# Kernel tuning notes

Measured on AMD Instinct MI355X. Metric: run time of the kernel, lower is better.

Reference implementation:

```python
import jax, jax.numpy as jnp
import numpy as np

B, P, T = 32, 196, 64
E = H = A = 512
V = 32000
L = 2  # num_layers


def _p(key, shape, scale=0.05):
    return jax.random.normal(key, shape, dtype=jnp.float32) * scale


def setup_inputs() -> dict:
    key = jax.random.key(0)
    ks = jax.random.split(key, 24)
    inp = {
        "encoder_out": jax.random.normal(ks[0], (B, P, E), dtype=jnp.float32),
        "captions": jax.random.randint(ks[1], (B, T), 0, V, dtype=jnp.int32),
        # embedding table (also tied fc weight)
        "emb_W": _p(ks[2], (V, E)),
        "fc_b": jnp.zeros((V,), jnp.float32),
        # attention
        "W_enc": _p(ks[3], (E, A)), "b_enc": jnp.zeros((A,), jnp.float32),
        "W_dec": _p(ks[4], (H, A)), "b_dec": jnp.zeros((A,), jnp.float32),
        "W_full": _p(ks[5], (A, 1)), "b_full": jnp.zeros((1,), jnp.float32),
        # LSTM layer 0 (input = 2E), layer 1 (input = H); PyTorch gate order i,f,g,o
        "Wih0": _p(ks[6], (4 * H, 2 * E)), "Whh0": _p(ks[7], (4 * H, H)),
        "bih0": jnp.zeros((4 * H,), jnp.float32), "bhh0": jnp.zeros((4 * H,), jnp.float32),
        "Wih1": _p(ks[8], (4 * H, H)), "Whh1": _p(ks[9], (4 * H, H)),
        "bih1": jnp.zeros((4 * H,), jnp.float32), "bhh1": jnp.zeros((4 * H,), jnp.float32),
        # init hidden/cell projections
        "W_init_h": _p(ks[10], (E, H * L)), "b_init_h": jnp.zeros((H * L,), jnp.float32),
        "W_init_c": _p(ks[11], (E, H * L)), "b_init_c": jnp.zeros((H * L,), jnp.float32),
    }
    return inp


def _lstm_cell(x, h, c, Wih, Whh, b):
    gates = x @ Wih.T + h @ Whh.T + b  # [B, 4H]
    i, f, g, o = jnp.split(gates, 4, axis=-1)
    c_new = jax.nn.sigmoid(f) * c + jax.nn.sigmoid(i) * jnp.tanh(g)
    h_new = jax.nn.sigmoid(o) * jnp.tanh(c_new)
    return h_new, c_new


def _forward(encoder_out, captions, emb_W, fc_b, W_enc, b_enc, W_dec, b_dec,
             W_full, b_full, Wih0, Whh0, bih0, bhh0, Wih1, Whh1, bih1, bhh1,
             W_init_h, b_init_h, W_init_c, b_init_c):
    # dropout is identity (eval mode)
    Bsz = encoder_out.shape[0]
    mean_enc = encoder_out.mean(axis=1)  # [B, E]
    # PyTorch: .view(num_layers, B, -1) on a [B, H*L] tensor -> flat reshape
    h = (mean_enc @ W_init_h + b_init_h).reshape(L, Bsz, H)
    c = (mean_enc @ W_init_c + b_init_c).reshape(L, Bsz, H)

    enc_att = encoder_out @ W_enc + b_enc  # [B, P, A] (timestep-invariant, hoisted)
    embs = emb_W[captions]  # [B, T, E]
    b0 = bih0 + bhh0
    b1 = bih1 + bhh1

    def step(carry, emb_t):
        h, c = carry  # each [L, B, H]
        att2 = h[-1] @ W_dec + b_dec  # [B, A]
        e = (jax.nn.relu(enc_att + att2[:, None, :]) @ W_full)[..., 0] + b_full[0]  # [B, P]
        alpha = jax.nn.softmax(e, axis=1)
        context = jnp.einsum('bp,bpe->be', alpha, encoder_out)  # [B, E]
        x = jnp.concatenate([emb_t, context], axis=-1)  # [B, 2E]
        h0, c0 = _lstm_cell(x, h[0], c[0], Wih0, Whh0, b0)
        h1, c1 = _lstm_cell(h0, h[1], c[1], Wih1, Whh1, b1)
        out = h1 @ emb_W.T + fc_b  # tied-weight projection [B, V]
        return (jnp.stack([h0, h1]), jnp.stack([c0, c1])), out

    (_, _), outs = jax.lax.scan(step, (h, c), jnp.swapaxes(embs, 0, 1))
    return jnp.swapaxes(outs, 0, 1)  # [B, T, V]


def reference(encoder_out, captions, emb_W, fc_b, W_enc, b_enc, W_dec, b_dec,
              W_full, b_full, Wih0, Whh0, bih0, bhh0, Wih1, Whh1, bih1, bhh1,
              W_init_h, b_init_h, W_init_c, b_init_c):
    return _forward(encoder_out, captions, emb_W, fc_b, W_enc, b_enc, W_dec, b_dec,
                    W_full, b_full, Wih0, Whh0, bih0, bhh0, Wih1, Whh1, bih1, bhh1,
                    W_init_h, b_init_h, W_init_c, b_init_c)
```

## Files before the change

### kernel.cpp

```cpp
#include <hip/hip_runtime.h>

typedef unsigned short u16;
typedef __attribute__((ext_vector_type(4))) float f32x4;
typedef __attribute__((ext_vector_type(2))) float f32x2;
typedef __attribute__((ext_vector_type(8))) short short8;

#define B_ 32
#define P_ 196
#define T_ 64
#define V_ 32000
#define SLABF 17408

#define AT_LOAD(p)     __hip_atomic_load((p), __ATOMIC_RELAXED, __HIP_MEMORY_SCOPE_AGENT)
#define AT_STORE(p,v)  __hip_atomic_store((p), (v), __ATOMIC_RELAXED, __HIP_MEMORY_SCOPE_AGENT)

__device__ __forceinline__ u16 f2bf(float x){
  unsigned int u = __float_as_uint(x);
  u += 0x7FFFu + ((u >> 16) & 1u);
  return (u16)(u >> 16);
}
__device__ __forceinline__ float bf2f(u16 x){
  return __uint_as_float(((unsigned int)x) << 16);
}
__device__ __forceinline__ float sigf(float x){ return 1.0f/(1.0f + __expf(-x)); }
__device__ __forceinline__ float tanhfast(float x){
  float e = __expf(-2.0f*fabsf(x));
  float t = (1.0f - e)/(1.0f + e);
  return x >= 0.0f ? t : -t;
}


__global__ __launch_bounds__(256) void k_cvt_bf16(const float* __restrict__ s,
                                                  u16* __restrict__ d, int n8){
  int i = blockIdx.x*256 + threadIdx.x;
  if (i >= n8) return;
  const f32x4* sp = (const f32x4*)(s + (size_t)i*8);
  f32x4 a = sp[0], b = sp[1];
  short8 v;
#pragma unroll
  for (int j=0;j<4;++j){ v[j] = (short)f2bf(a[j]); v[4+j] = (short)f2bf(b[j]); }
  *(short8*)(d + (size_t)i*8) = v;
}

__global__ __launch_bounds__(256) void k_wencT(const float* __restrict__ W, u16* __restrict__ WT){
  int tid = threadIdx.x;
  int kc = tid & 63, a = blockIdx.x*4 + (tid >> 6);
  short8 v;
#pragma unroll
  for (int j=0;j<8;++j) v[j] = (short)f2bf(W[(kc*8+j)*512 + a]);
  *(short8*)(WT + a*512 + kc*8) = v;
}

__global__ __launch_bounds__(256) void k_mean(const float* __restrict__ enc, float* __restrict__ mean){
  int b = blockIdx.x, tid = threadIdx.x;
  f32x2 acc; acc.x = 0.f; acc.y = 0.f;
  for (int p=0;p<P_;++p){
    f32x2 v = *(const f32x2*)(enc + ((size_t)(b*P_+p))*512 + tid*2);
    acc.x += v.x; acc.y += v.y;
  }
  acc.x *= (1.0f/196.0f); acc.y *= (1.0f/196.0f);
  *(f32x2*)(mean + b*512 + tid*2) = acc;
}

__global__ __launch_bounds__(256) void k_init_state(const float* __restrict__ mean,
    const float* __restrict__ Wh, const float* __restrict__ bh,
    const float* __restrict__ Wc, const float* __restrict__ bc,
    float* __restrict__ h0, float* __restrict__ h1,
    float* __restrict__ c0, float* __restrict__ c1){
  int bid = blockIdx.x;
  int which = bid >> 7, r = (bid >> 2) & 31, jg = bid & 3;
  const float* W = which ? Wc : Wh;
  const float* bb = which ? bc : bh;
  __shared__ float m[512];
  for (int i=threadIdx.x; i<512; i+=256) m[i] = mean[r*512 + i];
  __syncthreads();
  int j = jg*256 + threadIdx.x;
  float acc = bb[j];
  for (int e=0;e<512;++e) acc += m[e]*W[e*1024 + j];
  int l = r >> 4;
  int bb2 = ((r & 15) << 1) | (j >> 9);
  int hh = j & 511;
  float* dst = which ? (l ? c1 : c0) : (l ? h1 : h0);
  dst[bb2*512 + hh] = acc;
}

__global__ __launch_bounds__(256) void k_fuse_w(const float* __restrict__ Wih0,
    const float* __restrict__ Whh0, const float* __restrict__ Wih1,
    const float* __restrict__ Whh1, float* __restrict__ W0f, float* __restrict__ W1f){
  int r = blockIdx.x, tid = threadIdx.x;
  if (r < 2048){
    for (int k=tid; k<1536; k+=256)
      W0f[(size_t)r*1536+k] = (k<1024) ? Wih0[(size_t)r*1024+k] : Whh0[(size_t)r*512 + (k-1024)];
  } else {
    int r1 = r - 2048;
    for (int k=tid; k<1024; k+=256)
      W1f[(size_t)r1*1024+k] = (k<512) ? Wih1[(size_t)r1*512+k] : Whh1[(size_t)r1*512 + (k-512)];
  }
}

#define LDAP 40
__global__ __launch_bounds__(256) void k_gemm_bf16(
    const u16* __restrict__ A, const u16* __restrict__ Bm,
    const float* __restrict__ bias, float* __restrict__ C, int N){
  __shared__ __align__(16) u16 As[128*LDAP];
  __shared__ __align__(16) u16 Bs[128*LDAP];
  int tid = threadIdx.x, l = tid & 63, w = tid >> 6;
  int m0 = blockIdx.x * 128, n0 = blockIdx.y * 128;
  int wm = w >> 1, wn = w & 1;
  f32x4 acc[4][4];
#pragma unroll
  for (int a=0;a<4;++a)
#pragma unroll
    for (int b=0;b<4;++b) acc[a][b] = (f32x4)0.0f;
  int srow = tid >> 2, schunk = tid & 3;
  const u16* gA = A + (size_t)(m0 + srow)*512 + schunk*8;
  const u16* gB = Bm + (size_t)(n0 + srow)*512 + schunk*8;
  int lr = l & 15, lk = (l >> 4) * 8;
  for (int k0 = 0; k0 < 512; k0 += 32){
    short8 va0 = *(const short8*)(gA + k0);
    short8 va1 = *(const short8*)(gA + (size_t)64*512 + k0);
    short8 vb0 = *(const short8*)(gB + k0);
    short8 vb1 = *(const short8*)(gB + (size_t)64*512 + k0);
    __syncthreads();
    *(short8*)(As + srow*LDAP + schunk*8) = va0;
    *(short8*)(As + (64+srow)*LDAP + schunk*8) = va1;
    *(short8*)(Bs + srow*LDAP + schunk*8) = vb0;
    *(short8*)(Bs + (64+srow)*LDAP + schunk*8) = vb1;
    __syncthreads();
    short8 af[4], bfv[4];
#pragma unroll
    for (int mt=0; mt<4; ++mt) af[mt]  = *(const short8*)(As + (wm*64 + mt*16 + lr)*LDAP + lk);
#pragma unroll
    for (int nt=0; nt<4; ++nt) bfv[nt] = *(const short8*)(Bs + (wn*64 + nt*16 + lr)*LDAP + lk);
#pragma unroll
    for (int mt=0; mt<4; ++mt)
#pragma unroll
      for (int nt=0; nt<4; ++nt)
        acc[mt][nt] = __builtin_amdgcn_mfma_f32_16x16x32_bf16(af[mt], bfv[nt], acc[mt][nt], 0, 0, 0);
  }
#pragma unroll
  for (int mt=0; mt<4; ++mt){
    int row = m0 + wm*64 + mt*16 + ((l >> 4) << 2);
#pragma unroll
    for (int nt=0; nt<4; ++nt){
      int col = n0 + wn*64 + nt*16 + (l & 15);
      float bv = bias[col];
#pragma unroll
      for (int j=0;j<4;++j)
        C[(size_t)(row + j)*N + col] = acc[mt][nt][j] + bv;
    }
  }
}


struct RA {
  const float* enc; const int* caps; const float* embW;
  const u16* WdecBF; const float* bdec; const float* Wfull; const float* bfull;
  const u16* encattBF; const float* W0f; const float* W1f;
  const float* bih0; const float* bhh0; const float* bih1; const float* bhh1;
  float* h0g; float* h1g; float* att2g; float* ctxg;
  const float* c0init; const float* c1init;
  u16* h1_all; int* sync;
};

__device__ __forceinline__ void gbar(int* sync, int gen){
  __syncthreads();
  int tid = threadIdx.x;
  if (tid == 0) AT_STORE(&sync[blockIdx.x*32], gen);
  if (tid < 256 && tid != blockIdx.x){
    while (AT_LOAD(&sync[tid*32]) < gen) __builtin_amdgcn_s_sleep(4);
  }
  __syncthreads();
  asm volatile("" ::: "memory");
}

__global__ __launch_bounds__(512) void k_recur(RA a){
  int bid = blockIdx.x, tid = threadIdx.x;
  int lane = tid & 63, wv = tid >> 6;
  __shared__ __align__(16) float w0s[12288];
  __shared__ __align__(16) float w1s[8192];
  __shared__ float red[2048];
  __shared__ float c0s[64], c1s[64];
  __shared__ float SinvS;
  __shared__ int capl[32];

  int xcd = bid & 7;
  int ab = xcd*4 + ((bid >> 3) & 3);
  int as = bid >> 5, c0col = as*64;
  int bb = tid >> 4, ksg = tid & 15;

  for (int idx = tid; idx < 12288; idx += 512){
    int r = idx / 1536, rem = idx - r*1536;
    int ch = rem >> 9, rem2 = rem & 511;
    int q = rem2 >> 6, rem3 = rem2 & 63;
    int ks = rem3 >> 2, e = rem3 & 3;
    int grow = (r >> 1)*512 + bid*2 + (r & 1);
    w0s[idx] = a.W0f[(size_t)grow*1536 + ch*512 + ks*32 + q*4 + e];
  }
  for (int idx = tid; idx < 8192; idx += 512){
    int r = idx >> 10, rem = idx & 1023;
    int ch = rem >> 9, rem2 = rem & 511;
    int q = rem2 >> 6, rem3 = rem2 & 63;
    int ks = rem3 >> 2, e = rem3 & 3;
    int grow = (r >> 1)*512 + bid*2 + (r & 1);
    w1s[idx] = a.W1f[(size_t)grow*1024 + ch*512 + ks*32 + q*4 + e];
  }
  if (tid < 64){
    int ci = tid >> 5, b = tid & 31, cell = bid*2 + ci;
    c0s[ci*32+b] = a.c0init[b*512 + cell];
    c1s[ci*32+b] = a.c1init[b*512 + cell];
  }
  __syncthreads();

  for (int t = 0; t < T_; ++t){
    const float* h1_rd = a.h1g + (size_t)t*SLABF;
    const float* h0_rd = a.h0g + (size_t)t*SLABF;
    float*       h0_wr = a.h0g + (size_t)(t+1)*SLABF;
    float*       h1_wr = a.h1g + (size_t)(t+1)*SLABF;
    float*       at_wr = a.att2g + (size_t)t*SLABF;
    const float* at_rd = at_wr;
    float*       cx_wr = a.ctxg + (size_t)t*SLABF;
    const float* cx_rd = cx_wr;
    int genb = t*4;

    {
      float* h1s = red; float* gp = red + 512;
      h1s[tid] = h1_rd[ab*512 + tid];
      __syncthreads();
      int c = lane, ksx = wv;
      float accp = 0.f;
      const u16* wpd = a.WdecBF + (size_t)(ksx*64)*512 + c0col + c;
#pragma unroll 8
      for (int i=0;i<64;++i) accp = fmaf(h1s[ksx*64+i], bf2f(wpd[(size_t)i*512]), accp);
      gp[ksx*64+c] = accp;
      __syncthreads();
      if (tid < 64){
        float s = a.bdec[c0col+tid];
#pragma unroll
        for (int k=0;k<8;++k) s += gp[k*64+tid];
        AT_STORE(&at_wr[ab*512 + c0col + tid], s);
      }
    }
    gbar(a.sync, genb+1);

    {
      float* att2s = red; float* gp3 = red + 512; float* alph = red + 1024;
      att2s[tid] = at_rd[ab*512 + tid];
      __syncthreads();
      float a2[8], wf[8];
#pragma unroll
      for (int j=0;j<8;++j){ a2[j] = att2s[lane*8+j]; wf[j] = a.Wfull[lane*8+j]; }
      float bf0 = a.bfull[0];
      int np = (wv < 4) ? 25 : 24;
      for (int i=0;i<np;++i){
        int p = wv + i*8;
        const u16* ep = a.encattBF + ((size_t)(ab*P_ + p))*512 + lane*8;
        short8 ev = *(const short8*)ep;
        float s = 0.f;
#pragma unroll
        for (int j=0;j<8;++j)
          s += fmaxf(bf2f((u16)ev[j]) + a2[j], 0.f) * wf[j];
#pragma unroll
        for (int o=32;o>=1;o>>=1) s += __shfl_xor(s, o);
        if (lane == 0) alph[p] = __expf(s + bf0);
      }
      __syncthreads();
      if (wv == 0){
        float v = 0.f;
#pragma unroll
        for (int i=0;i<4;++i){ int p = lane + 64*i; if (p < P_) v += alph[p]; }
#pragma unroll
        for (int o=32;o>=1;o>>=1) v += __shfl_xor(v, o);
        if (lane == 0) SinvS = 1.0f / v;
      }
      int c = lane, pk = wv;
      float accp = 0.f;
      for (int i=0;i<25;++i){
        int p = pk + 8*i;
        if (p < P_) accp = fmaf(alph[p], a.enc[((size_t)(ab*P_ + p))*512 + c0col + c], accp);
      }
      gp3[pk*64+c] = accp;
      __syncthreads();
      if (tid < 64){
        float s = 0.f;
#pragma unroll
        for (int k=0;k<8;++k) s += gp3[k*64+tid];
        AT_STORE(&cx_wr[ab*512 + c0col + tid], s * SinvS);
      }
    }
    gbar(a.sync, genb+2);

    {
      if (tid < 32) capl[tid] = a.caps[tid*T_ + t];
      __syncthreads();
      float acc[8];
#pragma unroll
      for (int r=0;r<8;++r) acc[r] = 0.f;
#pragma unroll
      for (int ch=0; ch<3; ++ch){
        const float* src;
        if (ch == 0)      src = a.embW + (size_t)capl[bb]*512 + ksg*32;
        else if (ch == 1) src = cx_rd + bb*512 + ksg*32;
        else              src = h0_rd + bb*512 + ksg*32;
        f32x4 x[8];
#pragma unroll
        for (int q=0;q<8;++q) x[q] = *(const f32x4*)(src + q*4);
        const float* wb = w0s + ch*512 + ksg*4;
#pragma unroll
        for (int q=0;q<8;++q){
          f32x4 xq = x[q];
#pragma unroll
          for (int r=0;r<8;++r){
            f32x4 w4 = *(const f32x4*)(wb + r*1536 + q*64);
            acc[r] = fmaf(xq.x,w4.x, fmaf(xq.y,w4.y, fmaf(xq.z,w4.z, fmaf(xq.w,w4.w, acc[r]))));
          }
        }
      }
#pragma unroll
      for (int r=0;r<8;++r){
        float v = acc[r];
        v += __shfl_xor(v,1); v += __shfl_xor(v,2); v += __shfl_xor(v,4); v += __shfl_xor(v,8);
        acc[r] = v;
      }
      if (ksg == 0){
#pragma unroll
        for (int ci=0;ci<2;++ci){
          int cell = bid*2 + ci;
          float gi = acc[0+ci] + a.bih0[cell]        + a.bhh0[cell];
          float gf = acc[2+ci] + a.bih0[512+cell]    + a.bhh0[512+cell];
          float gg = acc[4+ci] + a.bih0[1024+cell]   + a.bhh0[1024+cell];
          float go = acc[6+ci] + a.bih0[1536+cell]   + a.bhh0[1536+cell];
          float cp = c0s[ci*32+bb];
          float cn = sigf(gf)*cp + sigf(gi)*tanhfast(gg);
          float hn = sigf(go)*tanhfast(cn);
          c0s[ci*32+bb] = cn;
          AT_STORE(&h0_wr[bb*512 + cell], hn);
        }
      }
    }
    gbar(a.sync, genb+3);

    {
      float acc[8];
#pragma unroll
      for (int r=0;r<8;++r) acc[r] = 0.f;
#pragma unroll
      for (int ch=0; ch<2; ++ch){
        const float* src = (ch == 0) ? (h0_wr + bb*512 + ksg*32)
                                     : (h1_rd + bb*512 + ksg*32);
        f32x4 x[8];
#pragma unroll
        for (int q=0;q<8;++q) x[q] = *(const f32x4*)(src + q*4);
        const float* wb = w1s + ch*512 + ksg*4;
#pragma unroll
        for (int q=0;q<8;++q){
          f32x4 xq = x[q];
#pragma unroll
          for (int r=0;r<8;++r){
            f32x4 w4 = *(const f32x4*)(wb + r*1024 + q*64);
            acc[r] = fmaf(xq.x,w4.x, fmaf(xq.y,w4.y, fmaf(xq.z,w4.z, fmaf(xq.w,w4.w, acc[r]))));
          }
        }
      }
#pragma unroll
      for (int r=0;r<8;++r){
        float v = acc[r];
        v += __shfl_xor(v,1); v += __shfl_xor(v,2); v += __shfl_xor(v,4); v += __shfl_xor(v,8);
        acc[r] = v;
      }
      if (ksg == 0){
#pragma unroll
        for (int ci=0;ci<2;++ci){
          int cell = bid*2 + ci;
          float gi = acc[0+ci] + a.bih1[cell]        + a.bhh1[cell];
          float gf = acc[2+ci] + a.bih1[512+cell]    + a.bhh1[512+cell];
          float gg = acc[4+ci] + a.bih1[1024+cell]   + a.bhh1[1024+cell];
          float go = acc[6+ci] + a.bih1[1536+cell]   + a.bhh1[1536+cell];
          float cp = c1s[ci*32+bb];
          float cn = sigf(gf)*cp + sigf(gi)*tanhfast(gg);
          float hn = sigf(go)*tanhfast(cn);
          c1s[ci*32+bb] = cn;
          AT_STORE(&h1_wr[bb*512 + cell], hn);
          a.h1_all[((size_t)(bb*T_ + t))*512 + cell] = f2bf(hn);
        }
      }
    }
    gbar(a.sync, genb+4);
  }
}


extern "C" void kernel_launch(void* const* d_in, const int* in_sizes, int n_in,
                              void* d_out, int out_size, void* d_ws, size_t ws_size,
                              hipStream_t stream){
  const float* enc   = (const float*)d_in[0];
  const int*   caps  = (const int*)d_in[1];
  const float* embW  = (const float*)d_in[2];
  const float* fc_b  = (const float*)d_in[3];
  const float* Wenc  = (const float*)d_in[4];
  const float* benc  = (const float*)d_in[5];
  const float* Wdec  = (const float*)d_in[6];
  const float* bdec  = (const float*)d_in[7];
  const float* Wfull = (const float*)d_in[8];
  const float* bfull = (const float*)d_in[9];
  const float* Wih0  = (const float*)d_in[10];
  const float* Whh0  = (const float*)d_in[11];
  const float* bih0  = (const float*)d_in[12];
  const float* bhh0  = (const float*)d_in[13];
  const float* Wih1  = (const float*)d_in[14];
  const float* Whh1  = (const float*)d_in[15];
  const float* bih1  = (const float*)d_in[16];
  const float* bhh1  = (const float*)d_in[17];
  const float* Winh  = (const float*)d_in[18];
  const float* binh  = (const float*)d_in[19];
  const float* Winc  = (const float*)d_in[20];
  const float* binc  = (const float*)d_in[21];
  float* out = (float*)d_out;

  char* wsp = (char*)d_ws;
  size_t off = 0;
  auto alloc = [&](size_t bytes)->char*{
    char* p = wsp + off;
    off += (bytes + 255) & ~(size_t)255;
    return p;
  };
  u16*   A_enc    = (u16*)  alloc((size_t)6272*512*2);
  u16*   emb_bf   = (u16*)  alloc((size_t)V_*512*2);
  u16*   WencT    = (u16*)  alloc((size_t)512*512*2);
  u16*   WdecBF   = (u16*)  alloc((size_t)512*512*2);
  float* encatt   = (float*)alloc((size_t)6272*512*4);
  u16*   encattBF = (u16*)  alloc((size_t)6272*512*2);
  float* meanb    = (float*)alloc((size_t)32*512*4);
  float* W0f      = (float*)alloc((size_t)2048*1536*4);
  float* W1f      = (float*)alloc((size_t)2048*1024*4);
  float* h0g      = (float*)alloc((size_t)65*SLABF*4);
  float* h1g      = (float*)alloc((size_t)65*SLABF*4);
  float* att2g    = (float*)alloc((size_t)65*SLABF*4);
  float* ctxg     = (float*)alloc((size_t)65*SLABF*4);
  float* c0init   = (float*)alloc(32*512*4);
  float* c1init   = (float*)alloc(32*512*4);
  u16*   h1_all   = (u16*)  alloc((size_t)2048*512*2);
  int*   syncA    = (int*)  alloc(8192*4);
  if (off > ws_size) return;

  hipMemsetAsync(syncA, 0, 8192*4, stream);
  k_cvt_bf16<<<1568, 256, 0, stream>>>(enc, A_enc, 401408);
  k_cvt_bf16<<<8000, 256, 0, stream>>>(embW, emb_bf, 2048000);
  k_cvt_bf16<<<128, 256, 0, stream>>>(Wdec, WdecBF, 32768);
  k_wencT   <<<128, 256, 0, stream>>>(Wenc, WencT);
  k_mean    <<<32, 256, 0, stream>>>(enc, meanb);
  k_init_state<<<256, 256, 0, stream>>>(meanb, Winh, binh, Winc, binc,
                                        h0g, h1g, c0init, c1init);
  k_fuse_w<<<4096, 256, 0, stream>>>(Wih0, Whh0, Wih1, Whh1, W0f, W1f);
  k_gemm_bf16<<<dim3(49, 4), 256, 0, stream>>>(A_enc, WencT, benc, encatt, 512);
  k_cvt_bf16<<<1568, 256, 0, stream>>>(encatt, encattBF, 401408);

  RA ra;
  ra.enc = enc; ra.caps = caps; ra.embW = embW;
  ra.WdecBF = WdecBF; ra.bdec = bdec; ra.Wfull = Wfull; ra.bfull = bfull;
  ra.encattBF = encattBF; ra.W0f = W0f; ra.W1f = W1f;
  ra.bih0 = bih0; ra.bhh0 = bhh0; ra.bih1 = bih1; ra.bhh1 = bhh1;
  ra.h0g = h0g; ra.h1g = h1g; ra.att2g = att2g; ra.ctxg = ctxg;
  ra.c0init = c0init; ra.c1init = c1init;
  ra.h1_all = h1_all; ra.sync = syncA;
  void* kp[] = { &ra };
  hipLaunchCooperativeKernel((const void*)k_recur, dim3(256), dim3(512), kp, 0, stream);

  k_gemm_bf16<<<dim3(16, 250), 256, 0, stream>>>(h1_all, emb_bf, fc_b, out, V_);
}
```

Measured before the change: 2.465 ms.

## Precompute off-critical-path LSTM partial gates in earlier phases, two batches per thread

The embedding part of the layer-0 gates and the h1-recurrent part of the layer-1 gates do not depend on the phase right before them. They are now computed early, in the att2 and context phases, and stored in shared memory (pa0/pa1). Only the context/h0 and h0 contributions stay on the critical path between barriers. The thread mapping also changes to 32 k-lanes by 2 batch rows per thread, so each LDS weight load is reused for two batches, and the weight smem layout is reordered to match. This shortens the serial work after gbar 2 and gbar 3 but adds work to the earlier phases and needs more registers.

```diff
diff --git a/kernel.cpp b/kernel.cpp
--- a/kernel.cpp
+++ b/kernel.cpp
@@ -180,6 +180,7 @@
   __shared__ __align__(16) float w0s[12288];
   __shared__ __align__(16) float w1s[8192];
   __shared__ float red[2048];
+  __shared__ float pa0[264], pa1[264];
   __shared__ float c0s[64], c1s[64];
   __shared__ float SinvS;
   __shared__ int capl[32];
@@ -187,23 +188,24 @@
   int xcd = bid & 7;
   int ab = xcd*4 + ((bid >> 3) & 3);
   int as = bid >> 5, c0col = as*64;
-  int bb = tid >> 4, ksg = tid & 15;
+  int bq = tid >> 5, ksg = tid & 31;
+  int b0 = bq*2, b1 = bq*2 + 1;
 
   for (int idx = tid; idx < 12288; idx += 512){
     int r = idx / 1536, rem = idx - r*1536;
     int ch = rem >> 9, rem2 = rem & 511;
-    int q = rem2 >> 6, rem3 = rem2 & 63;
+    int q = rem2 >> 7, rem3 = rem2 & 127;
     int ks = rem3 >> 2, e = rem3 & 3;
     int grow = (r >> 1)*512 + bid*2 + (r & 1);
-    w0s[idx] = a.W0f[(size_t)grow*1536 + ch*512 + ks*32 + q*4 + e];
+    w0s[idx] = a.W0f[(size_t)grow*1536 + ch*512 + ks*16 + q*4 + e];
   }
   for (int idx = tid; idx < 8192; idx += 512){
     int r = idx >> 10, rem = idx & 1023;
     int ch = rem >> 9, rem2 = rem & 511;
-    int q = rem2 >> 6, rem3 = rem2 & 63;
+    int q = rem2 >> 7, rem3 = rem2 & 127;
     int ks = rem3 >> 2, e = rem3 & 3;
     int grow = (r >> 1)*512 + bid*2 + (r & 1);
-    w1s[idx] = a.W1f[(size_t)grow*1024 + ch*512 + ks*32 + q*4 + e];
+    w1s[idx] = a.W1f[(size_t)grow*1024 + ch*512 + ks*16 + q*4 + e];
   }
   if (tid < 64){
     int ci = tid >> 5, b = tid & 31, cell = bid*2 + ci;
@@ -226,6 +228,7 @@
     {
       float* h1s = red; float* gp = red + 512;
       h1s[tid] = h1_rd[ab*512 + tid];
+      if (tid < 32) capl[tid] = a.caps[tid*T_ + t];
       __syncthreads();
       int c = lane, ksx = wv;
       float accp = 0.f;
@@ -241,6 +244,36 @@
         AT_STORE(&at_wr[ab*512 + c0col + tid], s);
       }
     }
+    {
+      float p0[8], p1[8];
+#pragma unroll
+      for (int r=0;r<8;++r){ p0[r]=0.f; p1[r]=0.f; }
+      const float* e0 = a.embW + (size_t)capl[b0]*512 + ksg*16;
+      const float* e1 = a.embW + (size_t)capl[b1]*512 + ksg*16;
+      f32x4 xa[4], xb[4];
+#pragma unroll
+      for (int q=0;q<4;++q){ xa[q] = *(const f32x4*)(e0 + q*4); xb[q] = *(const f32x4*)(e1 + q*4); }
+      const float* wb = w0s + ksg*4;
+#pragma unroll
+      for (int q=0;q<4;++q){
+        f32x4 x0 = xa[q], x1 = xb[q];
+#pragma unroll
+        for (int r=0;r<8;++r){
+          f32x4 w4 = *(const f32x4*)(wb + r*1536 + q*128);
+          p0[r] = fmaf(x0.x,w4.x, fmaf(x0.y,w4.y, fmaf(x0.z,w4.z, fmaf(x0.w,w4.w, p0[r]))));
+          p1[r] = fmaf(x1.x,w4.x, fmaf(x1.y,w4.y, fmaf(x1.z,w4.z, fmaf(x1.w,w4.w, p1[r]))));
+        }
+      }
+#pragma unroll
+      for (int r=0;r<8;++r){
+        float v0 = p0[r], v1 = p1[r];
+        v0 += __shfl_xor(v0,1); v0 += __shfl_xor(v0,2); v0 += __shfl_xor(v0,4);
+        v0 += __shfl_xor(v0,8); v0 += __shfl_xor(v0,16);
+        v1 += __shfl_xor(v1,1); v1 += __shfl_xor(v1,2); v1 += __shfl_xor(v1,4);
+        v1 += __shfl_xor(v1,8); v1 += __shfl_xor(v1,16);
+        if (ksg == 0){ pa0[r*33+b0] = v0; pa0[r*33+b1] = v1; }
+      }
+    }
     gbar(a.sync, genb+1);
 
     {
@@ -288,100 +321,161 @@
         AT_STORE(&cx_wr[ab*512 + c0col + tid], s * SinvS);
       }
     }
+    {
+      float p0[8], p1[8];
+#pragma unroll
+      for (int r=0;r<8;++r){ p0[r]=0.f; p1[r]=0.f; }
+      const float* s0 = h1_rd + b0*512 + ksg*16;
+      const float* s1 = h1_rd + b1*512 + ksg*16;
+      f32x4 xa[4], xb[4];
+#pragma unroll
+      for (int q=0;q<4;++q){ xa[q] = *(const f32x4*)(s0 + q*4); xb[q] = *(const f32x4*)(s1 + q*4); }
+      const float* wb = w1s + 512 + ksg*4;
+#pragma unroll
+      for (int q=0;q<4;++q){
+        f32x4 x0 = xa[q], x1 = xb[q];
+#pragma unroll
+        for (int r=0;r<8;++r){
+          f32x4 w4 = *(const f32x4*)(wb + r*1024 + q*128);
+          p0[r] = fmaf(x0.x,w4.x, fmaf(x0.y,w4.y, fmaf(x0.z,w4.z, fmaf(x0.w,w4.w, p0[r]))));
+          p1[r] = fmaf(x1.x,w4.x, fmaf(x1.y,w4.y, fmaf(x1.z,w4.z, fmaf(x1.w,w4.w, p1[r]))));
+        }
+      }
+#pragma unroll
+      for (int r=0;r<8;++r){
+        float v0 = p0[r], v1 = p1[r];
+        v0 += __shfl_xor(v0,1); v0 += __shfl_xor(v0,2); v0 += __shfl_xor(v0,4);
+        v0 += __shfl_xor(v0,8); v0 += __shfl_xor(v0,16);
+        v1 += __shfl_xor(v1,1); v1 += __shfl_xor(v1,2); v1 += __shfl_xor(v1,4);
+        v1 += __shfl_xor(v1,8); v1 += __shfl_xor(v1,16);
+        if (ksg == 0){ pa1[r*33+b0] = v0; pa1[r*33+b1] = v1; }
+      }
+    }
     gbar(a.sync, genb+2);
 
     {
-      if (tid < 32) capl[tid] = a.caps[tid*T_ + t];
-      __syncthreads();
-      float acc[8];
-#pragma unroll
-      for (int r=0;r<8;++r) acc[r] = 0.f;
-#pragma unroll
-      for (int ch=0; ch<3; ++ch){
-        const float* src;
-        if (ch == 0)      src = a.embW + (size_t)capl[bb]*512 + ksg*32;
-        else if (ch == 1) src = cx_rd + bb*512 + ksg*32;
-        else              src = h0_rd + bb*512 + ksg*32;
-        f32x4 x[8];
-#pragma unroll
-        for (int q=0;q<8;++q) x[q] = *(const f32x4*)(src + q*4);
-        const float* wb = w0s + ch*512 + ksg*4;
-#pragma unroll
-        for (int q=0;q<8;++q){
-          f32x4 xq = x[q];
+      float ac0[8], ac1[8];
+#pragma unroll
+      for (int r=0;r<8;++r){ ac0[r]=0.f; ac1[r]=0.f; }
+#pragma unroll
+      for (int ch=0; ch<2; ++ch){
+        const float* base = (ch == 0) ? cx_rd : h0_rd;
+        const float* s0 = base + b0*512 + ksg*16;
+        const float* s1 = base + b1*512 + ksg*16;
+        f32x4 xa[4], xb[4];
+#pragma unroll
+        for (int q=0;q<4;++q){ xa[q] = *(const f32x4*)(s0 + q*4); xb[q] = *(const f32x4*)(s1 + q*4); }
+        const float* wb = w0s + (ch+1)*512 + ksg*4;
+#pragma unroll
+        for (int q=0;q<4;++q){
+          f32x4 x0 = xa[q], x1 = xb[q];
 #pragma unroll
           for (int r=0;r<8;++r){
-            f32x4 w4 = *(const f32x4*)(wb + r*1536 + q*64);
-            acc[r] = fmaf(xq.x,w4.x, fmaf(xq.y,w4.y, fmaf(xq.z,w4.z, fmaf(xq.w,w4.w, acc[r]))));
+            f32x4 w4 = *(const f32x4*)(wb + r*1536 + q*128);
+            ac0[r] = fmaf(x0.x,w4.x, fmaf(x0.y,w4.y, fmaf(x0.z,w4.z, fmaf(x0.w,w4.w, ac0[r]))));
+            ac1[r] = fmaf(x1.x,w4.x, fmaf(x1.y,w4.y, fmaf(x1.z,w4.z, fmaf(x1.w,w4.w, ac1[r]))));
           }
         }
       }
 #pragma unroll
       for (int r=0;r<8;++r){
-        float v = acc[r];
-        v += __shfl_xor(v,1); v += __shfl_xor(v,2); v += __shfl_xor(v,4); v += __shfl_xor(v,8);
-        acc[r] = v;
+        float v0 = ac0[r], v1 = ac1[r];
+        v0 += __shfl_xor(v0,1); v0 += __shfl_xor(v0,2); v0 += __shfl_xor(v0,4);
+        v0 += __shfl_xor(v0,8); v0 += __shfl_xor(v0,16);
+        v1 += __shfl_xor(v1,1); v1 += __shfl_xor(v1,2); v1 += __shfl_xor(v1,4);
+        v1 += __shfl_xor(v1,8); v1 += __shfl_xor(v1,16);
+        ac0[r] = v0; ac1[r] = v1;
       }
       if (ksg == 0){
 #pragma unroll
         for (int ci=0;ci<2;++ci){
           int cell = bid*2 + ci;
-          float gi = acc[0+ci] + a.bih0[cell]        + a.bhh0[cell];
-          float gf = acc[2+ci] + a.bih0[512+cell]    + a.bhh0[512+cell];
-          float gg = acc[4+ci] + a.bih0[1024+cell]   + a.bhh0[1024+cell];
-          float go = acc[6+ci] + a.bih0[1536+cell]   + a.bhh0[1536+cell];
-          float cp = c0s[ci*32+bb];
-          float cn = sigf(gf)*cp + sigf(gi)*tanhfast(gg);
-          float hn = sigf(go)*tanhfast(cn);
-          c0s[ci*32+bb] = cn;
-          AT_STORE(&h0_wr[bb*512 + cell], hn);
-        }
-      }
-    }
-    gbar(a.sync, genb+3);
-
-    {
-      float acc[8];
-#pragma unroll
-      for (int r=0;r<8;++r) acc[r] = 0.f;
-#pragma unroll
-      for (int ch=0; ch<2; ++ch){
-        const float* src = (ch == 0) ? (h0_wr + bb*512 + ksg*32)
-                                     : (h1_rd + bb*512 + ksg*32);
-        f32x4 x[8];
-#pragma unroll
-        for (int q=0;q<8;++q) x[q] = *(const f32x4*)(src + q*4);
-        const float* wb = w1s + ch*512 + ksg*4;
-#pragma unroll
-        for (int q=0;q<8;++q){
-          f32x4 xq = x[q];
-#pragma unroll
-          for (int r=0;r<8;++r){
-            f32x4 w4 = *(const f32x4*)(wb + r*1024 + q*64);
-            acc[r] = fmaf(xq.x,w4.x, fmaf(xq.y,w4.y, fmaf(xq.z,w4.z, fmaf(xq.w,w4.w, acc[r]))));
+          {
+            float gi = ac0[0+ci] + pa0[(0+ci)*33+b0] + a.bih0[cell]      + a.bhh0[cell];
+            float gf = ac0[2+ci] + pa0[(2+ci)*33+b0] + a.bih0[512+cell]  + a.bhh0[512+cell];
+            float gg = ac0[4+ci] + pa0[(4+ci)*33+b0] + a.bih0[1024+cell] + a.bhh0[1024+cell];
+            float go = ac0[6+ci] + pa0[(6+ci)*33+b0] + a.bih0[1536+cell] + a.bhh0[1536+cell];
+            float cp = c0s[ci*32+b0];
+            float cn = sigf(gf)*cp + sigf(gi)*tanhfast(gg);
+            float hn = sigf(go)*tanhfast(cn);
+            c0s[ci*32+b0] = cn;
+            AT_STORE(&h0_wr[b0*512 + cell], hn);
+          }
+          {
+            float gi = ac1[0+ci] + pa0[(0+ci)*33+b1] + a.bih0[cell]      + a.bhh0[cell];
+            float gf = ac1[2+ci] + pa0[(2+ci)*33+b1] + a.bih0[512+cell]  + a.bhh0[512+cell];
+            float gg = ac1[4+ci] + pa0[(4+ci)*33+b1] + a.bih0[1024+cell] + a.bhh0[1024+cell];
+            float go = ac1[6+ci] + pa0[(6+ci)*33+b1] + a.bih0[1536+cell] + a.bhh0[1536+cell];
+            float cp = c0s[ci*32+b1];
+            float cn = sigf(gf)*cp + sigf(gi)*tanhfast(gg);
+            float hn = sigf(go)*tanhfast(cn);
+            c0s[ci*32+b1] = cn;
+            AT_STORE(&h0_wr[b1*512 + cell], hn);
           }
         }
       }
+    }
+    gbar(a.sync, genb+3);
+
+    {
+      float ac0[8], ac1[8];
+#pragma unroll
+      for (int r=0;r<8;++r){ ac0[r]=0.f; ac1[r]=0.f; }
+      {
+        const float* s0 = h0_wr + b0*512 + ksg*16;
+        const float* s1 = h0_wr + b1*512 + ksg*16;
+        f32x4 xa[4], xb[4];
+#pragma unroll
+        for (int q=0;q<4;++q){ xa[q] = *(const f32x4*)(s0 + q*4); xb[q] = *(const f32x4*)(s1 + q*4); }
+        const float* wb = w1s + ksg*4;
+#pragma unroll
+        for (int q=0;q<4;++q){
+          f32x4 x0 = xa[q], x1 = xb[q];
+#pragma unroll
+          for (int r=0;r<8;++r){
+            f32x4 w4 = *(const f32x4*)(wb + r*1024 + q*128);
+            ac0[r] = fmaf(x0.x,w4.x, fmaf(x0.y,w4.y, fmaf(x0.z,w4.z, fmaf(x0.w,w4.w, ac0[r]))));
+            ac1[r] = fmaf(x1.x,w4.x, fmaf(x1.y,w4.y, fmaf(x1.z,w4.z, fmaf(x1.w,w4.w, ac1[r]))));
+          }
+        }
+      }
 #pragma unroll
       for (int r=0;r<8;++r){
-        float v = acc[r];
-        v += __shfl_xor(v,1); v += __shfl_xor(v,2); v += __shfl_xor(v,4); v += __shfl_xor(v,8);
-        acc[r] = v;
+        float v0 = ac0[r], v1 = ac1[r];
+        v0 += __shfl_xor(v0,1); v0 += __shfl_xor(v0,2); v0 += __shfl_xor(v0,4);
+        v0 += __shfl_xor(v0,8); v0 += __shfl_xor(v0,16);
+        v1 += __shfl_xor(v1,1); v1 += __shfl_xor(v1,2); v1 += __shfl_xor(v1,4);
+        v1 += __shfl_xor(v1,8); v1 += __shfl_xor(v1,16);
+        ac0[r] = v0; ac1[r] = v1;
       }
       if (ksg == 0){
 #pragma unroll
         for (int ci=0;ci<2;++ci){
           int cell = bid*2 + ci;
-          float gi = acc[0+ci] + a.bih1[cell]        + a.bhh1[cell];
-          float gf = acc[2+ci] + a.bih1[512+cell]    + a.bhh1[512+cell];
-          float gg = acc[4+ci] + a.bih1[1024+cell]   + a.bhh1[1024+cell];
-          float go = acc[6+ci] + a.bih1[1536+cell]   + a.bhh1[1536+cell];
-          float cp = c1s[ci*32+bb];
-          float cn = sigf(gf)*cp + sigf(gi)*tanhfast(gg);
-          float hn = sigf(go)*tanhfast(cn);
-          c1s[ci*32+bb] = cn;
-          AT_STORE(&h1_wr[bb*512 + cell], hn);
-          a.h1_all[((size_t)(bb*T_ + t))*512 + cell] = f2bf(hn);
+          {
+            float gi = ac0[0+ci] + pa1[(0+ci)*33+b0] + a.bih1[cell]      + a.bhh1[cell];
+            float gf = ac0[2+ci] + pa1[(2+ci)*33+b0] + a.bih1[512+cell]  + a.bhh1[512+cell];
+            float gg = ac0[4+ci] + pa1[(4+ci)*33+b0] + a.bih1[1024+cell] + a.bhh1[1024+cell];
+            float go = ac0[6+ci] + pa1[(6+ci)*33+b0] + a.bih1[1536+cell] + a.bhh1[1536+cell];
+            float cp = c1s[ci*32+b0];
+            float cn = sigf(gf)*cp + sigf(gi)*tanhfast(gg);
+            float hn = sigf(go)*tanhfast(cn);
+            c1s[ci*32+b0] = cn;
+            AT_STORE(&h1_wr[b0*512 + cell], hn);
+            a.h1_all[((size_t)(b0*T_ + t))*512 + cell] = f2bf(hn);
+          }
+          {
+            float gi = ac1[0+ci] + pa1[(0+ci)*33+b1] + a.bih1[cell]      + a.bhh1[cell];
+            float gf = ac1[2+ci] + pa1[(2+ci)*33+b1] + a.bih1[512+cell]  + a.bhh1[512+cell];
+            float gg = ac1[4+ci] + pa1[(4+ci)*33+b1] + a.bih1[1024+cell] + a.bhh1[1024+cell];
+            float go = ac1[6+ci] + pa1[(6+ci)*33+b1] + a.bih1[1536+cell] + a.bhh1[1536+cell];
+            float cp = c1s[ci*32+b1];
+            float cn = sigf(gf)*cp + sigf(gi)*tanhfast(gg);
+            float hn = sigf(go)*tanhfast(cn);
+            c1s[ci*32+b1] = cn;
+            AT_STORE(&h1_wr[b1*512 + cell], hn);
+            a.h1_all[((size_t)(b1*T_ + t))*512 + cell] = f2bf(hn);
+          }
         }
       }
     }
```

New measurement: 2.732 ms. 10.8% more time.

## Partition recurrent kernel per batch row with 8-block group barriers and bf16 streamed weights

Applied to the files above, without the earlier changes.

The persistent recurrent kernel is restructured so each batch row is owned by a group of 8 blocks that split the hidden cells. Grid-wide 256-block barriers are replaced by 8-block group barriers. LSTM weights are packed into bf16 and streamed from global memory (L2) each step instead of being held as fp32 in LDS. The attention softmax gains a cross-block exp exchange, and context reads the bf16 encoder copy. This is meant to cut global barrier latency, but each block now rereads about 2.5 MB of weights per step and accepts extra bf16 rounding.

```diff
diff --git a/kernel.cpp b/kernel.cpp
--- a/kernel.cpp
+++ b/kernel.cpp
@@ -10,6 +10,7 @@
 #define T_ 64
 #define V_ 32000
 #define SLABF 17408
+#define EXPS  7424
 
 #define AT_LOAD(p)     __hip_atomic_load((p), __ATOMIC_RELAXED, __HIP_MEMORY_SCOPE_AGENT)
 #define AT_STORE(p,v)  __hip_atomic_store((p), (v), __ATOMIC_RELAXED, __HIP_MEMORY_SCOPE_AGENT)
@@ -84,17 +85,24 @@
   dst[bb2*512 + hh] = acc;
 }
 
-__global__ __launch_bounds__(256) void k_fuse_w(const float* __restrict__ Wih0,
+__global__ __launch_bounds__(512) void k_pack(const float* __restrict__ Wih0,
     const float* __restrict__ Whh0, const float* __restrict__ Wih1,
-    const float* __restrict__ Whh1, float* __restrict__ W0f, float* __restrict__ W1f){
-  int r = blockIdx.x, tid = threadIdx.x;
-  if (r < 2048){
-    for (int k=tid; k<1536; k+=256)
-      W0f[(size_t)r*1536+k] = (k<1024) ? Wih0[(size_t)r*1024+k] : Whh0[(size_t)r*512 + (k-1024)];
+    const float* __restrict__ Whh1, u16* __restrict__ W0bf, u16* __restrict__ W1bf){
+  int bidx = blockIdx.x, tid = threadIdx.x;
+  int ci = tid >> 3, e = tid & 7;
+  if (bidx < 6144){
+    int kc = bidx % 192, gg = bidx / 192;
+    int gate = gg & 3, g = gg >> 2;
+    int row = gate*512 + g*64 + ci, k = kc*8 + e;
+    float v = (k < 1024) ? Wih0[(size_t)row*1024 + k] : Whh0[(size_t)row*512 + (k-1024)];
+    W0bf[(size_t)bidx*512 + tid] = f2bf(v);
   } else {
-    int r1 = r - 2048;
-    for (int k=tid; k<1024; k+=256)
-      W1f[(size_t)r1*1024+k] = (k<512) ? Wih1[(size_t)r1*512+k] : Whh1[(size_t)r1*512 + (k-512)];
+    int b2 = bidx - 6144;
+    int kc = b2 % 128, gg = b2 / 128;
+    int gate = gg & 3, g = gg >> 2;
+    int row = gate*512 + g*64 + ci, k = kc*8 + e;
+    float v = (k < 512) ? Wih1[(size_t)row*512 + k] : Whh1[(size_t)row*512 + (k-512)];
+    W1bf[(size_t)b2*512 + tid] = f2bf(v);
   }
 }
 
@@ -154,63 +162,41 @@
 
 
 struct RA {
-  const float* enc; const int* caps; const float* embW;
-  const u16* WdecBF; const float* bdec; const float* Wfull; const float* bfull;
-  const u16* encattBF; const float* W0f; const float* W1f;
+  const int* caps; const float* embW; const float* Wdec; const float* bdec;
+  const float* Wfull; const float* bfull;
+  const u16* encattBF; const u16* encBF;
+  const u16* W0bf; const u16* W1bf;
   const float* bih0; const float* bhh0; const float* bih1; const float* bhh1;
-  float* h0g; float* h1g; float* att2g; float* ctxg;
+  float* h0g; float* h1g; float* att2g; float* ctxg; float* expg;
   const float* c0init; const float* c1init;
   u16* h1_all; int* sync;
 };
 
-__device__ __forceinline__ void gbar(int* sync, int gen){
-  __syncthreads();
-  int tid = threadIdx.x;
-  if (tid == 0) AT_STORE(&sync[blockIdx.x*32], gen);
-  if (tid < 256 && tid != blockIdx.x){
-    while (AT_LOAD(&sync[tid*32]) < gen) __builtin_amdgcn_s_sleep(4);
-  }
-  __syncthreads();
-  asm volatile("" ::: "memory");
-}
-
 __global__ __launch_bounds__(512) void k_recur(RA a){
   int bid = blockIdx.x, tid = threadIdx.x;
   int lane = tid & 63, wv = tid >> 6;
-  __shared__ __align__(16) float w0s[12288];
-  __shared__ __align__(16) float w1s[8192];
+  int b = bid >> 3, g = bid & 7;
+
+  __shared__ __align__(16) float xs[1536];
   __shared__ float red[2048];
+  __shared__ float alph[224];
   __shared__ float c0s[64], c1s[64];
   __shared__ float SinvS;
-  __shared__ int capl[32];
-
-  int xcd = bid & 7;
-  int ab = xcd*4 + ((bid >> 3) & 3);
-  int as = bid >> 5, c0col = as*64;
-  int bb = tid >> 4, ksg = tid & 15;
-
-  for (int idx = tid; idx < 12288; idx += 512){
-    int r = idx / 1536, rem = idx - r*1536;
-    int ch = rem >> 9, rem2 = rem & 511;
-    int q = rem2 >> 6, rem3 = rem2 & 63;
-    int ks = rem3 >> 2, e = rem3 & 3;
-    int grow = (r >> 1)*512 + bid*2 + (r & 1);
-    w0s[idx] = a.W0f[(size_t)grow*1536 + ch*512 + ks*32 + q*4 + e];
-  }
-  for (int idx = tid; idx < 8192; idx += 512){
-    int r = idx >> 10, rem = idx & 1023;
-    int ch = rem >> 9, rem2 = rem & 511;
-    int q = rem2 >> 6, rem3 = rem2 & 63;
-    int ks = rem3 >> 2, e = rem3 & 3;
-    int grow = (r >> 1)*512 + bid*2 + (r & 1);
-    w1s[idx] = a.W1f[(size_t)grow*1024 + ch*512 + ks*32 + q*4 + e];
-  }
+  __shared__ int capS;
+
   if (tid < 64){
-    int ci = tid >> 5, b = tid & 31, cell = bid*2 + ci;
-    c0s[ci*32+b] = a.c0init[b*512 + cell];
-    c1s[ci*32+b] = a.c1init[b*512 + cell];
+    c0s[tid] = a.c0init[b*512 + g*64 + tid];
+    c1s[tid] = a.c1init[b*512 + g*64 + tid];
   }
   __syncthreads();
+
+  int* gf = a.sync;
+#define GRPBAR(gen_) { \
+    __syncthreads(); \
+    if (tid == 0) AT_STORE(&gf[(b*8 + g)*32], (gen_)); \
+    if (tid < 8){ while (AT_LOAD(&gf[(b*8 + tid)*32]) < (gen_)) __builtin_amdgcn_s_sleep(1); } \
+    __syncthreads(); \
+    asm volatile("" ::: "memory"); }
 
   for (int t = 0; t < T_; ++t){
     const float* h1_rd = a.h1g + (size_t)t*SLABF;
@@ -221,172 +207,195 @@
     const float* at_rd = at_wr;
     float*       cx_wr = a.ctxg + (size_t)t*SLABF;
     const float* cx_rd = cx_wr;
-    int genb = t*4;
+    float*       ex_wr = a.expg + (size_t)t*EXPS;
+    const float* ex_rd = ex_wr;
+    int gen0 = t*5;
+
+    if (tid == 0) capS = a.caps[b*T_ + t];
+    __syncthreads();
+    xs[tid] = a.embW[(size_t)capS*512 + tid];
 
     {
       float* h1s = red; float* gp = red + 512;
-      h1s[tid] = h1_rd[ab*512 + tid];
-      __syncthreads();
-      int c = lane, ksx = wv;
-      float accp = 0.f;
-      const u16* wpd = a.WdecBF + (size_t)(ksx*64)*512 + c0col + c;
+      h1s[tid] = h1_rd[b*512 + tid];
+      __syncthreads();
+      float acc = 0.f;
+      const float* wpd = a.Wdec + (size_t)(wv*64)*512 + g*64 + lane;
 #pragma unroll 8
-      for (int i=0;i<64;++i) accp = fmaf(h1s[ksx*64+i], bf2f(wpd[(size_t)i*512]), accp);
-      gp[ksx*64+c] = accp;
+      for (int i=0;i<64;++i) acc = fmaf(h1s[wv*64+i], wpd[(size_t)i*512], acc);
+      gp[wv*64+lane] = acc;
       __syncthreads();
       if (tid < 64){
-        float s = a.bdec[c0col+tid];
+        float s = a.bdec[g*64+tid];
 #pragma unroll
         for (int k=0;k<8;++k) s += gp[k*64+tid];
-        AT_STORE(&at_wr[ab*512 + c0col + tid], s);
-      }
-    }
-    gbar(a.sync, genb+1);
+        AT_STORE(&at_wr[b*512 + g*64 + tid], s);
+      }
+    }
+    GRPBAR(gen0+1);
 
     {
-      float* att2s = red; float* gp3 = red + 512; float* alph = red + 1024;
-      att2s[tid] = at_rd[ab*512 + tid];
+      float* att2s = red;
+      att2s[tid] = at_rd[b*512 + tid];
       __syncthreads();
       float a2[8], wf[8];
 #pragma unroll
       for (int j=0;j<8;++j){ a2[j] = att2s[lane*8+j]; wf[j] = a.Wfull[lane*8+j]; }
       float bf0 = a.bfull[0];
-      int np = (wv < 4) ? 25 : 24;
-      for (int i=0;i<np;++i){
-        int p = wv + i*8;
-        const u16* ep = a.encattBF + ((size_t)(ab*P_ + p))*512 + lane*8;
-        short8 ev = *(const short8*)ep;
-        float s = 0.f;
-#pragma unroll
-        for (int j=0;j<8;++j)
-          s += fmaxf(bf2f((u16)ev[j]) + a2[j], 0.f) * wf[j];
-#pragma unroll
-        for (int o=32;o>=1;o>>=1) s += __shfl_xor(s, o);
-        if (lane == 0) alph[p] = __expf(s + bf0);
-      }
+      int np = (g < 4) ? 25 : 24;
+      int base = (g < 4) ? g*25 : 100 + (g-4)*24;
+      for (int i=0;i<4;++i){
+        int is = wv + i*8;
+        if (is < np){
+          int p = base + is;
+          const u16* ep = a.encattBF + ((size_t)(b*P_ + p))*512 + lane*8;
+          short8 ev = *(const short8*)ep;
+          float s = 0.f;
+#pragma unroll
+          for (int j=0;j<8;++j)
+            s += fmaxf(bf2f((u16)ev[j]) + a2[j], 0.f) * wf[j];
+#pragma unroll
+          for (int o=32;o>=1;o>>=1) s += __shfl_xor(s, o);
+          if (lane == 0) AT_STORE(&ex_wr[b*224 + p], __expf(s + bf0));
+        }
+      }
+    }
+    GRPBAR(gen0+2);
+
+    {
+      if (tid < 224) alph[tid] = (tid < P_) ? ex_rd[b*224 + tid] : 0.f;
       __syncthreads();
       if (wv == 0){
         float v = 0.f;
 #pragma unroll
-        for (int i=0;i<4;++i){ int p = lane + 64*i; if (p < P_) v += alph[p]; }
+        for (int i=0;i<4;++i){ int idx = lane + 64*i; if (idx < 224) v += alph[idx]; }
 #pragma unroll
         for (int o=32;o>=1;o>>=1) v += __shfl_xor(v, o);
         if (lane == 0) SinvS = 1.0f / v;
       }
-      int c = lane, pk = wv;
-      float accp = 0.f;
+      __syncthreads();
+      float* gp = red + 512;
+      float acc = 0.f;
       for (int i=0;i<25;++i){
-        int p = pk + 8*i;
-        if (p < P_) accp = fmaf(alph[p], a.enc[((size_t)(ab*P_ + p))*512 + c0col + c], accp);
-      }
-      gp3[pk*64+c] = accp;
+        int p = wv + 8*i;
+        if (p < P_)
+          acc = fmaf(alph[p], bf2f(a.encBF[((size_t)(b*P_ + p))*512 + g*64 + lane]), acc);
+      }
+      gp[wv*64+lane] = acc;
       __syncthreads();
       if (tid < 64){
         float s = 0.f;
 #pragma unroll
-        for (int k=0;k<8;++k) s += gp3[k*64+tid];
-        AT_STORE(&cx_wr[ab*512 + c0col + tid], s * SinvS);
-      }
-    }
-    gbar(a.sync, genb+2);
+        for (int k=0;k<8;++k) s += gp[k*64+tid];
+        AT_STORE(&cx_wr[b*512 + g*64 + tid], s * SinvS);
+      }
+    }
+    GRPBAR(gen0+3);
 
     {
-      if (tid < 32) capl[tid] = a.caps[tid*T_ + t];
-      __syncthreads();
-      float acc[8];
-#pragma unroll
-      for (int r=0;r<8;++r) acc[r] = 0.f;
-#pragma unroll
-      for (int ch=0; ch<3; ++ch){
-        const float* src;
-        if (ch == 0)      src = a.embW + (size_t)capl[bb]*512 + ksg*32;
-        else if (ch == 1) src = cx_rd + bb*512 + ksg*32;
-        else              src = h0_rd + bb*512 + ksg*32;
-        f32x4 x[8];
-#pragma unroll
-        for (int q=0;q<8;++q) x[q] = *(const f32x4*)(src + q*4);
-        const float* wb = w0s + ch*512 + ksg*4;
-#pragma unroll
-        for (int q=0;q<8;++q){
-          f32x4 xq = x[q];
-#pragma unroll
-          for (int r=0;r<8;++r){
-            f32x4 w4 = *(const f32x4*)(wb + r*1536 + q*64);
-            acc[r] = fmaf(xq.x,w4.x, fmaf(xq.y,w4.y, fmaf(xq.z,w4.z, fmaf(xq.w,w4.w, acc[r]))));
-          }
+      xs[512 + tid]  = cx_rd[b*512 + tid];
+      xs[1024 + tid] = h0_rd[b*512 + tid];
+      __syncthreads();
+      float ac[4];
+#pragma unroll
+      for (int r=0;r<4;++r) ac[r] = 0.f;
+      const u16* w0base = a.W0bf + ((size_t)(g*4)*192)*512 + lane*8;
+#pragma unroll 4
+      for (int j=0;j<24;++j){
+        int kc = wv*24 + j;
+        f32x4 xlo = *(const f32x4*)&xs[kc*8];
+        f32x4 xhi = *(const f32x4*)&xs[kc*8+4];
+#pragma unroll
+        for (int gate=0; gate<4; ++gate){
+          short8 w8 = *(const short8*)(w0base + ((size_t)(gate*192 + kc))*512);
+          float s = ac[gate];
+          s = fmaf(bf2f((u16)w8[0]), xlo.x, s);
+          s = fmaf(bf2f((u16)w8[1]), xlo.y, s);
+          s = fmaf(bf2f((u16)w8[2]), xlo.z, s);
+          s = fmaf(bf2f((u16)w8[3]), xlo.w, s);
+          s = fmaf(bf2f((u16)w8[4]), xhi.x, s);
+          s = fmaf(bf2f((u16)w8[5]), xhi.y, s);
+          s = fmaf(bf2f((u16)w8[6]), xhi.z, s);
+          s = fmaf(bf2f((u16)w8[7]), xhi.w, s);
+          ac[gate] = s;
         }
       }
-#pragma unroll
-      for (int r=0;r<8;++r){
-        float v = acc[r];
-        v += __shfl_xor(v,1); v += __shfl_xor(v,2); v += __shfl_xor(v,4); v += __shfl_xor(v,8);
-        acc[r] = v;
-      }
-      if (ksg == 0){
-#pragma unroll
-        for (int ci=0;ci<2;++ci){
-          int cell = bid*2 + ci;
-          float gi = acc[0+ci] + a.bih0[cell]        + a.bhh0[cell];
-          float gf = acc[2+ci] + a.bih0[512+cell]    + a.bhh0[512+cell];
-          float gg = acc[4+ci] + a.bih0[1024+cell]   + a.bhh0[1024+cell];
-          float go = acc[6+ci] + a.bih0[1536+cell]   + a.bhh0[1536+cell];
-          float cp = c0s[ci*32+bb];
-          float cn = sigf(gf)*cp + sigf(gi)*tanhfast(gg);
-          float hn = sigf(go)*tanhfast(cn);
-          c0s[ci*32+bb] = cn;
-          AT_STORE(&h0_wr[bb*512 + cell], hn);
+      __syncthreads();
+#pragma unroll
+      for (int gate=0; gate<4; ++gate) red[(gate*8 + wv)*64 + lane] = ac[gate];
+      __syncthreads();
+      if (tid < 64){
+        int cell = g*64 + tid;
+        float G[4];
+#pragma unroll
+        for (int gate=0; gate<4; ++gate){
+          float s = a.bih0[gate*512+cell] + a.bhh0[gate*512+cell];
+#pragma unroll
+          for (int ks=0; ks<8; ++ks) s += red[(gate*8+ks)*64 + tid];
+          G[gate] = s;
         }
-      }
-    }
-    gbar(a.sync, genb+3);
+        float cp = c0s[tid];
+        float cn = sigf(G[1])*cp + sigf(G[0])*tanhfast(G[2]);
+        float hn = sigf(G[3])*tanhfast(cn);
+        c0s[tid] = cn;
+        AT_STORE(&h0_wr[b*512 + cell], hn);
+      }
+    }
+    GRPBAR(gen0+4);
 
     {
-      float acc[8];
-#pragma unroll
-      for (int r=0;r<8;++r) acc[r] = 0.f;
-#pragma unroll
-      for (int ch=0; ch<2; ++ch){
-        const float* src = (ch == 0) ? (h0_wr + bb*512 + ksg*32)
-                                     : (h1_rd + bb*512 + ksg*32);
-        f32x4 x[8];
-#pragma unroll
-        for (int q=0;q<8;++q) x[q] = *(const f32x4*)(src + q*4);
-        const float* wb = w1s + ch*512 + ksg*4;
-#pragma unroll
-        for (int q=0;q<8;++q){
-          f32x4 xq = x[q];
-#pragma unroll
-          for (int r=0;r<8;++r){
-            f32x4 w4 = *(const f32x4*)(wb + r*1024 + q*64);
-            acc[r] = fmaf(xq.x,w4.x, fmaf(xq.y,w4.y, fmaf(xq.z,w4.z, fmaf(xq.w,w4.w, acc[r]))));
-          }
+      xs[tid]       = h0_wr[b*512 + tid];
+      xs[512 + tid] = h1_rd[b*512 + tid];
+      __syncthreads();
+      float ac[4];
+#pragma unroll
+      for (int r=0;r<4;++r) ac[r] = 0.f;
+      const u16* w1base = a.W1bf + ((size_t)(g*4)*128)*512 + lane*8;
+#pragma unroll 4
+      for (int j=0;j<16;++j){
+        int kc = wv*16 + j;
+        f32x4 xlo = *(const f32x4*)&xs[kc*8];
+        f32x4 xhi = *(const f32x4*)&xs[kc*8+4];
+#pragma unroll
+        for (int gate=0; gate<4; ++gate){
+          short8 w8 = *(const short8*)(w1base + ((size_t)(gate*128 + kc))*512);
+          float s = ac[gate];
+          s = fmaf(bf2f((u16)w8[0]), xlo.x, s);
+          s = fmaf(bf2f((u16)w8[1]), xlo.y, s);
+          s = fmaf(bf2f((u16)w8[2]), xlo.z, s);
+          s = fmaf(bf2f((u16)w8[3]), xlo.w, s);
+          s = fmaf(bf2f((u16)w8[4]), xhi.x, s);
+          s = fmaf(bf2f((u16)w8[5]), xhi.y, s);
+          s = fmaf(bf2f((u16)w8[6]), xhi.z, s);
+          s = fmaf(bf2f((u16)w8[7]), xhi.w, s);
+          ac[gate] = s;
         }
       }
-#pragma unroll
-      for (int r=0;r<8;++r){
-        float v = acc[r];
-        v += __shfl_xor(v,1); v += __shfl_xor(v,2); v += __shfl_xor(v,4); v += __shfl_xor(v,8);
-        acc[r] = v;
-      }
-      if (ksg == 0){
-#pragma unroll
-        for (int ci=0;ci<2;++ci){
-          int cell = bid*2 + ci;
-          float gi = acc[0+ci] + a.bih1[cell]        + a.bhh1[cell];
-          float gf = acc[2+ci] + a.bih1[512+cell]    + a.bhh1[512+cell];
-          float gg = acc[4+ci] + a.bih1[1024+cell]   + a.bhh1[1024+cell];
-          float go = acc[6+ci] + a.bih1[1536+cell]   + a.bhh1[1536+cell];
-          float cp = c1s[ci*32+bb];
-          float cn = sigf(gf)*cp + sigf(gi)*tanhfast(gg);
-          float hn = sigf(go)*tanhfast(cn);
-          c1s[ci*32+bb] = cn;
-          AT_STORE(&h1_wr[bb*512 + cell], hn);
-          a.h1_all[((size_t)(bb*T_ + t))*512 + cell] = f2bf(hn);
+      __syncthreads();
+#pragma unroll
+      for (int gate=0; gate<4; ++gate) red[(gate*8 + wv)*64 + lane] = ac[gate];
+      __syncthreads();
+      if (tid < 64){
+        int cell = g*64 + tid;
+        float G[4];
+#pragma unroll
+        for (int gate=0; gate<4; ++gate){
+          float s = a.bih1[gate*512+cell] + a.bhh1[gate*512+cell];
+#pragma unroll
+          for (int ks=0; ks<8; ++ks) s += red[(gate*8+ks)*64 + tid];
+          G[gate] = s;
         }
-      }
-    }
-    gbar(a.sync, genb+4);
-  }
+        float cp = c1s[tid];
+        float cn = sigf(G[1])*cp + sigf(G[0])*tanhfast(G[2]);
+        float hn = sigf(G[3])*tanhfast(cn);
+        c1s[tid] = cn;
+        AT_STORE(&h1_wr[b*512 + cell], hn);
+        a.h1_all[((size_t)(b*T_ + t))*512 + cell] = f2bf(hn);
+      }
+    }
+    GRPBAR(gen0+5);
+  }
+#undef GRPBAR
 }
 
 
@@ -427,16 +436,16 @@
   u16*   A_enc    = (u16*)  alloc((size_t)6272*512*2);
   u16*   emb_bf   = (u16*)  alloc((size_t)V_*512*2);
   u16*   WencT    = (u16*)  alloc((size_t)512*512*2);
-  u16*   WdecBF   = (u16*)  alloc((size_t)512*512*2);
   float* encatt   = (float*)alloc((size_t)6272*512*4);
   u16*   encattBF = (u16*)  alloc((size_t)6272*512*2);
   float* meanb    = (float*)alloc((size_t)32*512*4);
-  float* W0f      = (float*)alloc((size_t)2048*1536*4);
-  float* W1f      = (float*)alloc((size_t)2048*1024*4);
+  u16*   W0bf     = (u16*)  alloc((size_t)2048*1536*2);
+  u16*   W1bf     = (u16*)  alloc((size_t)2048*1024*2);
   float* h0g      = (float*)alloc((size_t)65*SLABF*4);
   float* h1g      = (float*)alloc((size_t)65*SLABF*4);
   float* att2g    = (float*)alloc((size_t)65*SLABF*4);
   float* ctxg     = (float*)alloc((size_t)65*SLABF*4);
+  float* expg     = (float*)alloc((size_t)65*EXPS*4);
   float* c0init   = (float*)alloc(32*512*4);
   float* c1init   = (float*)alloc(32*512*4);
   u16*   h1_all   = (u16*)  alloc((size_t)2048*512*2);
@@ -446,21 +455,21 @@
   hipMemsetAsync(syncA, 0, 8192*4, stream);
   k_cvt_bf16<<<1568, 256, 0, stream>>>(enc, A_enc, 401408);
   k_cvt_bf16<<<8000, 256, 0, stream>>>(embW, emb_bf, 2048000);
-  k_cvt_bf16<<<128, 256, 0, stream>>>(Wdec, WdecBF, 32768);
   k_wencT   <<<128, 256, 0, stream>>>(Wenc, WencT);
   k_mean    <<<32, 256, 0, stream>>>(enc, meanb);
   k_init_state<<<256, 256, 0, stream>>>(meanb, Winh, binh, Winc, binc,
                                         h0g, h1g, c0init, c1init);
-  k_fuse_w<<<4096, 256, 0, stream>>>(Wih0, Whh0, Wih1, Whh1, W0f, W1f);
+  k_pack<<<10240, 512, 0, stream>>>(Wih0, Whh0, Wih1, Whh1, W0bf, W1bf);
   k_gemm_bf16<<<dim3(49, 4), 256, 0, stream>>>(A_enc, WencT, benc, encatt, 512);
   k_cvt_bf16<<<1568, 256, 0, stream>>>(encatt, encattBF, 401408);
 
   RA ra;
-  ra.enc = enc; ra.caps = caps; ra.embW = embW;
-  ra.WdecBF = WdecBF; ra.bdec = bdec; ra.Wfull = Wfull; ra.bfull = bfull;
-  ra.encattBF = encattBF; ra.W0f = W0f; ra.W1f = W1f;
+  ra.caps = caps; ra.embW = embW; ra.Wdec = Wdec; ra.bdec = bdec;
+  ra.Wfull = Wfull; ra.bfull = bfull;
+  ra.encattBF = encattBF; ra.encBF = A_enc;
+  ra.W0bf = W0bf; ra.W1bf = W1bf;
   ra.bih0 = bih0; ra.bhh0 = bhh0; ra.bih1 = bih1; ra.bhh1 = bhh1;
-  ra.h0g = h0g; ra.h1g = h1g; ra.att2g = att2g; ra.ctxg = ctxg;
+  ra.h0g = h0g; ra.h1g = h1g; ra.att2g = att2g; ra.ctxg = ctxg; ra.expg = expg;
   ra.c0init = c0init; ra.c1init = c1init;
   ra.h1_all = h1_all; ra.sync = syncA;
   void* kp[] = { &ra };
```

Measured after the change: 2.756 ms. 1.12x slower.
